# Kernel tuning notes

Hardware: AMD Instinct MI355X
Metric: run time of the kernel (lower is better)

The kernel has to match this reference:

```python
import jax, jax.numpy as jnp
import numpy as np

# Normalized sobel kernels (kornia normalize_kernel2d: divide by abs-sum = 8)
_SOBEL = np.array([
    [[-1., 0., 1.], [-2., 0., 2.], [-1., 0., 1.]],   # d/dx
    [[-1., -2., -1.], [0., 0., 0.], [1., 2., 1.]],   # d/dy
], dtype=np.float32) / 8.0
_EPS = 1e-6


def _rgb_to_grayscale(x):
    # kornia weights; x: [B,3,H,W] -> [B,1,H,W]
    return 0.299 * x[:, 0:1] + 0.587 * x[:, 1:2] + 0.114 * x[:, 2:3]


def _sobel_edges(x):
    gray = _rgb_to_grayscale(x)
    # replicate padding of 1 (kornia spatial_gradient uses replicate)
    p = jnp.pad(gray, ((0, 0), (0, 0), (1, 1), (1, 1)), mode='edge')
    k = jnp.asarray(_SOBEL)[:, None]  # [2,1,3,3] OIHW
    g = jax.lax.conv_general_dilated(
        p, k, window_strides=(1, 1), padding='VALID',
        dimension_numbers=('NCHW', 'OIHW', 'NCHW'))  # [B,2,H,W]
    # gradient magnitude: sqrt(gx^2 + gy^2 + eps)
    return jnp.sqrt(jnp.sum(g * g, axis=1, keepdims=True) + _EPS)  # [B,1,H,W]


def setup_inputs() -> dict:
    key = jax.random.key(0)
    k1, k2 = jax.random.split(key)
    shape = (16, 3, 512, 512)
    prediction = jax.random.uniform(k1, shape, dtype=jnp.float32)
    target = jax.random.uniform(k2, shape, dtype=jnp.float32)
    return {"prediction": prediction, "target": target}


def reference(prediction, target):
    # forward runs under torch.no_grad() in the original module
    pe = jax.lax.stop_gradient(_sobel_edges(prediction))
    te = jax.lax.stop_gradient(_sobel_edges(target))
    return jnp.mean(jnp.abs(pe - te))  # l1_loss, mean reduction
```

## Files before the change

kernel.cpp:

```cpp
#include <hip/hip_runtime.h>


constexpr int B = 16;
constexpr int H = 512;
constexpr int W = 512;
constexpr int TH = 32;
constexpr int TW = 64;
constexpr int HALO_H = TH + 2;
constexpr int HALO_W = TW + 2;
constexpr int NTHREADS = 256;
constexpr int TILES_W = W / TW;
constexpr int TILES_H = H / TH;
constexpr int TILES_PER_IMG = TILES_W * TILES_H;
constexpr int NBLOCKS = B * TILES_PER_IMG;
constexpr float EPS = 1e-6f;

__device__ __forceinline__ float gray_at(const float* __restrict__ img, int h, int w) {
    const float* p = img + (size_t)h * W + w;
    const size_t plane = (size_t)H * W;
    return 0.299f * p[0] + 0.587f * p[plane] + 0.114f * p[2 * plane];
}

__global__ __launch_bounds__(NTHREADS) void edge_loss_kernel(
    const float* __restrict__ pred,
    const float* __restrict__ targ,
    float* __restrict__ out)
{
    __shared__ float sp[HALO_H][HALO_W];
    __shared__ float st[HALO_H][HALO_W];

    const int bid = blockIdx.x;
    const int b   = bid / TILES_PER_IMG;
    const int t   = bid % TILES_PER_IMG;
    const int th0 = (t / TILES_W) * TH;
    const int tw0 = (t % TILES_W) * TW;
    const int tid = threadIdx.x;

    const float* __restrict__ pimg = pred + (size_t)b * 3 * H * W;
    const float* __restrict__ timg = targ + (size_t)b * 3 * H * W;

    for (int i = tid; i < HALO_H * HALO_W; i += NTHREADS) {
        const int lh = i / HALO_W;
        const int lw = i - lh * HALO_W;
        const int gh = min(max(th0 + lh - 1, 0), H - 1);
        const int gw = min(max(tw0 + lw - 1, 0), W - 1);
        sp[lh][lw] = gray_at(pimg, gh, gw);
        st[lh][lw] = gray_at(timg, gh, gw);
    }
    __syncthreads();

    float acc = 0.0f;
    #pragma unroll
    for (int r = 0; r < (TH * TW) / NTHREADS; ++r) {
        const int i  = tid + r * NTHREADS;
        const int lh = i >> 6;
        const int lw = i & 63;

        {
            const float p00 = sp[lh    ][lw], p01 = sp[lh    ][lw + 1], p02 = sp[lh    ][lw + 2];
            const float p10 = sp[lh + 1][lw],                            p12 = sp[lh + 1][lw + 2];
            const float p20 = sp[lh + 2][lw], p21 = sp[lh + 2][lw + 1], p22 = sp[lh + 2][lw + 2];
            const float gx = 0.125f * ((p02 - p00) + 2.0f * (p12 - p10) + (p22 - p20));
            const float gy = 0.125f * ((p20 - p00) + 2.0f * (p21 - p01) + (p22 - p02));
            const float pe = sqrtf(gx * gx + gy * gy + EPS);

            const float q00 = st[lh    ][lw], q01 = st[lh    ][lw + 1], q02 = st[lh    ][lw + 2];
            const float q10 = st[lh + 1][lw],                            q12 = st[lh + 1][lw + 2];
            const float q20 = st[lh + 2][lw], q21 = st[lh + 2][lw + 1], q22 = st[lh + 2][lw + 2];
            const float hx = 0.125f * ((q02 - q00) + 2.0f * (q12 - q10) + (q22 - q20));
            const float hy = 0.125f * ((q20 - q00) + 2.0f * (q21 - q01) + (q22 - q02));
            const float te = sqrtf(hx * hx + hy * hy + EPS);

            acc += fabsf(pe - te);
        }
    }

    #pragma unroll
    for (int off = 32; off > 0; off >>= 1)
        acc += __shfl_down(acc, off);

    __shared__ float wsum[NTHREADS / 64];
    if ((tid & 63) == 0) wsum[tid >> 6] = acc;
    __syncthreads();

    if (tid == 0) {
        float s = wsum[0] + wsum[1] + wsum[2] + wsum[3];
        atomicAdd(out, s * (1.0f / (float)((size_t)B * H * W)));
    }
}

extern "C" void kernel_launch(void* const* d_in, const int* in_sizes, int n_in,
                              void* d_out, int out_size, void* d_ws, size_t ws_size,
                              hipStream_t stream) {
    const float* pred = (const float*)d_in[0];
    const float* targ = (const float*)d_in[1];
    float* out = (float*)d_out;

    hipMemsetAsync(out, 0, sizeof(float), stream);
    edge_loss_kernel<<<NBLOCKS, NTHREADS, 0, stream>>>(pred, targ, out);
}
```

Before: 139.1 us.

## Vectorize halo loads with float4 and slide stencil rows in registers

Measured after the change: 134.6 us. 1.03x faster.

```diff
diff --git a/kernel.cpp b/kernel.cpp
--- a/kernel.cpp
+++ b/kernel.cpp
@@ -6,19 +6,18 @@
 constexpr int W = 512;
 constexpr int TH = 32;
 constexpr int TW = 64;
-constexpr int HALO_H = TH + 2;
-constexpr int HALO_W = TW + 2;
+constexpr int HROWS = TH + 2;
+constexpr int LSTRIDE = 72;
 constexpr int NTHREADS = 256;
 constexpr int TILES_W = W / TW;
 constexpr int TILES_H = H / TH;
 constexpr int TILES_PER_IMG = TILES_W * TILES_H;
 constexpr int NBLOCKS = B * TILES_PER_IMG;
+constexpr int NGRP = HROWS * (TW / 4);
 constexpr float EPS = 1e-6f;
 
-__device__ __forceinline__ float gray_at(const float* __restrict__ img, int h, int w) {
-    const float* p = img + (size_t)h * W + w;
-    const size_t plane = (size_t)H * W;
-    return 0.299f * p[0] + 0.587f * p[plane] + 0.114f * p[2 * plane];
+__device__ __forceinline__ float4 ldg4(const float* p) {
+    return *reinterpret_cast<const float4*>(p);
 }
 
 __global__ __launch_bounds__(NTHREADS) void edge_loss_kernel(
@@ -26,8 +25,8 @@
     const float* __restrict__ targ,
     float* __restrict__ out)
 {
-    __shared__ float sp[HALO_H][HALO_W];
-    __shared__ float st[HALO_H][HALO_W];
+    __shared__ alignas(16) float sp[HROWS][LSTRIDE];
+    __shared__ alignas(16) float st[HROWS][LSTRIDE];
 
     const int bid = blockIdx.x;
     const int b   = bid / TILES_PER_IMG;
@@ -35,44 +34,81 @@
     const int th0 = (t / TILES_W) * TH;
     const int tw0 = (t % TILES_W) * TW;
     const int tid = threadIdx.x;
+    const size_t plane = (size_t)H * W;
 
-    const float* __restrict__ pimg = pred + (size_t)b * 3 * H * W;
-    const float* __restrict__ timg = targ + (size_t)b * 3 * H * W;
+    const float* __restrict__ pimg = pred + (size_t)b * 3 * plane;
+    const float* __restrict__ timg = targ + (size_t)b * 3 * plane;
 
-    for (int i = tid; i < HALO_H * HALO_W; i += NTHREADS) {
-        const int lh = i / HALO_W;
-        const int lw = i - lh * HALO_W;
-        const int gh = min(max(th0 + lh - 1, 0), H - 1);
-        const int gw = min(max(tw0 + lw - 1, 0), W - 1);
-        sp[lh][lw] = gray_at(pimg, gh, gw);
-        st[lh][lw] = gray_at(timg, gh, gw);
+    for (int g = tid; g < NGRP; g += NTHREADS) {
+        const int row  = g >> 4;
+        const int k    = g & 15;
+        const int grow = min(max(th0 - 1 + row, 0), H - 1);
+        const float* pp = pimg + (size_t)grow * W + (tw0 + 4 * k);
+        const float* tp = timg + (size_t)grow * W + (tw0 + 4 * k);
+        const float4 pr = ldg4(pp);
+        const float4 pg = ldg4(pp + plane);
+        const float4 pb = ldg4(pp + 2 * plane);
+        const float4 tr = ldg4(tp);
+        const float4 tg = ldg4(tp + plane);
+        const float4 tb = ldg4(tp + 2 * plane);
+        float4 gp, gt;
+        gp.x = 0.299f * pr.x + 0.587f * pg.x + 0.114f * pb.x;
+        gp.y = 0.299f * pr.y + 0.587f * pg.y + 0.114f * pb.y;
+        gp.z = 0.299f * pr.z + 0.587f * pg.z + 0.114f * pb.z;
+        gp.w = 0.299f * pr.w + 0.587f * pg.w + 0.114f * pb.w;
+        gt.x = 0.299f * tr.x + 0.587f * tg.x + 0.114f * tb.x;
+        gt.y = 0.299f * tr.y + 0.587f * tg.y + 0.114f * tb.y;
+        gt.z = 0.299f * tr.z + 0.587f * tg.z + 0.114f * tb.z;
+        gt.w = 0.299f * tr.w + 0.587f * tg.w + 0.114f * tb.w;
+        *reinterpret_cast<float4*>(&sp[row][4 + 4 * k]) = gp;
+        *reinterpret_cast<float4*>(&st[row][4 + 4 * k]) = gt;
+    }
+
+    if (tid < 4 * HROWS) {
+        const int img  = tid & 1;
+        const int rr   = tid >> 1;
+        const int side = rr >= HROWS;
+        const int row  = side ? rr - HROWS : rr;
+        const int grow = min(max(th0 - 1 + row, 0), H - 1);
+        const int gcol = side ? min(tw0 + TW, W - 1) : max(tw0 - 1, 0);
+        const float* ip = (img ? timg : pimg) + (size_t)grow * W + gcol;
+        const float v = 0.299f * ip[0] + 0.587f * ip[plane] + 0.114f * ip[2 * plane];
+        float (*dst)[LSTRIDE] = img ? st : sp;
+        dst[row][side ? 68 : 3] = v;
     }
     __syncthreads();
 
+    const int lw = tid & 63;
+    const int q  = tid >> 6;
+    const int r0 = q * 8;
+    const int c0 = lw + 3, c1 = lw + 4, c2 = lw + 5;
+
+    float pa0 = sp[r0][c0],     pa1 = sp[r0][c1],     pa2 = sp[r0][c2];
+    float pb0 = sp[r0 + 1][c0], pb1 = sp[r0 + 1][c1], pb2 = sp[r0 + 1][c2];
+    float ta0 = st[r0][c0],     ta1 = st[r0][c1],     ta2 = st[r0][c2];
+    float tb0 = st[r0 + 1][c0], tb1 = st[r0 + 1][c1], tb2 = st[r0 + 1][c2];
+
     float acc = 0.0f;
     #pragma unroll
-    for (int r = 0; r < (TH * TW) / NTHREADS; ++r) {
-        const int i  = tid + r * NTHREADS;
-        const int lh = i >> 6;
-        const int lw = i & 63;
+    for (int r = 0; r < 8; ++r) {
+        const int hr = r0 + r + 2;
+        const float pc0 = sp[hr][c0], pc1 = sp[hr][c1], pc2 = sp[hr][c2];
+        const float tc0 = st[hr][c0], tc1 = st[hr][c1], tc2 = st[hr][c2];
 
-        {
-            const float p00 = sp[lh    ][lw], p01 = sp[lh    ][lw + 1], p02 = sp[lh    ][lw + 2];
-            const float p10 = sp[lh + 1][lw],                            p12 = sp[lh + 1][lw + 2];
-            const float p20 = sp[lh + 2][lw], p21 = sp[lh + 2][lw + 1], p22 = sp[lh + 2][lw + 2];
-            const float gx = 0.125f * ((p02 - p00) + 2.0f * (p12 - p10) + (p22 - p20));
-            const float gy = 0.125f * ((p20 - p00) + 2.0f * (p21 - p01) + (p22 - p02));
-            const float pe = sqrtf(gx * gx + gy * gy + EPS);
+        float gx = ((pa2 - pa0) + 2.0f * (pb2 - pb0) + (pc2 - pc0)) * 0.125f;
+        float gy = ((pc0 - pa0) + 2.0f * (pc1 - pa1) + (pc2 - pa2)) * 0.125f;
+        const float pe = sqrtf(gx * gx + gy * gy + EPS);
 
-            const float q00 = st[lh    ][lw], q01 = st[lh    ][lw + 1], q02 = st[lh    ][lw + 2];
-            const float q10 = st[lh + 1][lw],                            q12 = st[lh + 1][lw + 2];
-            const float q20 = st[lh + 2][lw], q21 = st[lh + 2][lw + 1], q22 = st[lh + 2][lw + 2];
-            const float hx = 0.125f * ((q02 - q00) + 2.0f * (q12 - q10) + (q22 - q20));
-            const float hy = 0.125f * ((q20 - q00) + 2.0f * (q21 - q01) + (q22 - q02));
-            const float te = sqrtf(hx * hx + hy * hy + EPS);
+        float hx = ((ta2 - ta0) + 2.0f * (tb2 - tb0) + (tc2 - tc0)) * 0.125f;
+        float hy = ((tc0 - ta0) + 2.0f * (tc1 - ta1) + (tc2 - ta2)) * 0.125f;
+        const float te = sqrtf(hx * hx + hy * hy + EPS);
 
-            acc += fabsf(pe - te);
-        }
+        acc += fabsf(pe - te);
+
+        pa0 = pb0; pa1 = pb1; pa2 = pb2;
+        pb0 = pc0; pb1 = pc1; pb2 = pc2;
+        ta0 = tb0; ta1 = tb1; ta2 = tb2;
+        tb0 = tc0; tb1 = tc1; tb2 = tc2;
     }
 
     #pragma unroll
@@ -84,7 +120,7 @@
     __syncthreads();
 
     if (tid == 0) {
-        float s = wsum[0] + wsum[1] + wsum[2] + wsum[3];
+        const float s = wsum[0] + wsum[1] + wsum[2] + wsum[3];
         atomicAdd(out, s * (1.0f / (float)((size_t)B * H * W)));
     }
 }
```

## Replace shared-memory tiles with register-sliding wave strips and separable Sobel

Applied to the files above, without the earlier changes.

Measured after the change: 131.3 us. 5.6% less time.

```diff
diff --git a/kernel.cpp b/kernel.cpp
--- a/kernel.cpp
+++ b/kernel.cpp
@@ -4,88 +4,153 @@
 constexpr int B = 16;
 constexpr int H = 512;
 constexpr int W = 512;
-constexpr int TH = 32;
-constexpr int TW = 64;
-constexpr int HALO_H = TH + 2;
-constexpr int HALO_W = TW + 2;
+constexpr int PLANE = H * W;
+constexpr int SR = 8;
 constexpr int NTHREADS = 256;
-constexpr int TILES_W = W / TW;
-constexpr int TILES_H = H / TH;
-constexpr int TILES_PER_IMG = TILES_W * TILES_H;
-constexpr int NBLOCKS = B * TILES_PER_IMG;
+constexpr int WAVES_PER_BLOCK = NTHREADS / 64;
+constexpr int STRIPS = B * 2 * (H / SR);
+constexpr int NBLOCKS = STRIPS / WAVES_PER_BLOCK;
 constexpr float EPS = 1e-6f;
 
-__device__ __forceinline__ float gray_at(const float* __restrict__ img, int h, int w) {
-    const float* p = img + (size_t)h * W + w;
-    const size_t plane = (size_t)H * W;
-    return 0.299f * p[0] + 0.587f * p[plane] + 0.114f * p[2 * plane];
+__device__ __forceinline__ float4 ldg4(const float* p) {
+    return *reinterpret_cast<const float4*>(p);
 }
 
-__global__ __launch_bounds__(NTHREADS) void edge_loss_kernel(
+__device__ __forceinline__ float4 gray4(float4 r, float4 g, float4 b) {
+    float4 o;
+    o.x = 0.299f * r.x + 0.587f * g.x + 0.114f * b.x;
+    o.y = 0.299f * r.y + 0.587f * g.y + 0.114f * b.y;
+    o.z = 0.299f * r.z + 0.587f * g.z + 0.114f * b.z;
+    o.w = 0.299f * r.w + 0.587f * g.w + 0.114f * b.w;
+    return o;
+}
+
+struct DS { float4 D, S; };
+
+__device__ __forceinline__ DS load_row(
+    const float* __restrict__ x0, const float* __restrict__ x1,
+    const float* __restrict__ x2,
+    int row, int col, int ecol, int lane)
+{
+    const int off = row * W + col;
+    const float4 r = ldg4(x0 + off);
+    const float4 g = ldg4(x1 + off);
+    const float4 b = ldg4(x2 + off);
+
+    float e = 0.0f;
+    if ((lane == 0) | (lane == 63)) {
+        const int eo = row * W + ecol;
+        e = 0.299f * x0[eo] + 0.587f * x1[eo] + 0.114f * x2[eo];
+    }
+
+    const float4 G = gray4(r, g, b);
+    float left  = __shfl_up(G.w, 1);
+    float right = __shfl_down(G.x, 1);
+    if (lane == 0)  left  = e;
+    if (lane == 63) right = e;
+
+    DS o;
+    o.D.x = G.y - left;
+    o.D.y = G.z - G.x;
+    o.D.z = G.w - G.y;
+    o.D.w = right - G.z;
+    o.S.x = left + 2.0f * G.x + G.y;
+    o.S.y = G.x  + 2.0f * G.y + G.z;
+    o.S.z = G.y  + 2.0f * G.z + G.w;
+    o.S.w = G.z  + 2.0f * G.w + right;
+    return o;
+}
+
+__device__ __forceinline__ float px_loss(
+    float dm, float d0, float dp, float sm, float sp,
+    float em, float e0, float ep, float qm, float qp)
+{
+    const float gx = (dm + 2.0f * d0 + dp) * 0.125f;
+    const float gy = (sp - sm) * 0.125f;
+    const float pe = sqrtf(gx * gx + gy * gy + EPS);
+    const float hx = (em + 2.0f * e0 + ep) * 0.125f;
+    const float hy = (qp - qm) * 0.125f;
+    const float te = sqrtf(hx * hx + hy * hy + EPS);
+    return fabsf(pe - te);
+}
+
+__global__ __launch_bounds__(NTHREADS, 2) void edge_loss_kernel(
     const float* __restrict__ pred,
     const float* __restrict__ targ,
-    float* __restrict__ out)
+    float* __restrict__ partial)
 {
-    __shared__ float sp[HALO_H][HALO_W];
-    __shared__ float st[HALO_H][HALO_W];
+    const int tid  = threadIdx.x;
+    const int lane = tid & 63;
+    const int s    = blockIdx.x * WAVES_PER_BLOCK + (tid >> 6);
+    const int img  = s >> 7;
+    const int half = (s >> 6) & 1;
+    const int vs   = s & 63;
+    const int r0   = vs * SR;
+    const int c0   = half * 256;
+    const int col  = c0 + 4 * lane;
+    const int ecol = (lane == 0) ? max(c0 - 1, 0) : min(c0 + 256, W - 1);
 
-    const int bid = blockIdx.x;
-    const int b   = bid / TILES_PER_IMG;
-    const int t   = bid % TILES_PER_IMG;
-    const int th0 = (t / TILES_W) * TH;
-    const int tw0 = (t % TILES_W) * TW;
-    const int tid = threadIdx.x;
+    const float* __restrict__ p0 = pred + (size_t)img * 3 * PLANE;
+    const float* __restrict__ p1 = p0 + PLANE;
+    const float* __restrict__ p2 = p0 + 2 * PLANE;
+    const float* __restrict__ t0 = targ + (size_t)img * 3 * PLANE;
+    const float* __restrict__ t1 = t0 + PLANE;
+    const float* __restrict__ t2 = t0 + 2 * PLANE;
 
-    const float* __restrict__ pimg = pred + (size_t)b * 3 * H * W;
-    const float* __restrict__ timg = targ + (size_t)b * 3 * H * W;
-
-    for (int i = tid; i < HALO_H * HALO_W; i += NTHREADS) {
-        const int lh = i / HALO_W;
-        const int lw = i - lh * HALO_W;
-        const int gh = min(max(th0 + lh - 1, 0), H - 1);
-        const int gw = min(max(tw0 + lw - 1, 0), W - 1);
-        sp[lh][lw] = gray_at(pimg, gh, gw);
-        st[lh][lw] = gray_at(timg, gh, gw);
-    }
-    __syncthreads();
+    const int rm = max(r0 - 1, 0);
+    DS pm = load_row(p0, p1, p2, rm, col, ecol, lane);
+    DS tm = load_row(t0, t1, t2, rm, col, ecol, lane);
+    DS pc = load_row(p0, p1, p2, r0, col, ecol, lane);
+    DS tc = load_row(t0, t1, t2, r0, col, ecol, lane);
 
     float acc = 0.0f;
     #pragma unroll
-    for (int r = 0; r < (TH * TW) / NTHREADS; ++r) {
-        const int i  = tid + r * NTHREADS;
-        const int lh = i >> 6;
-        const int lw = i & 63;
+    for (int r = 0; r < SR; ++r) {
+        const int rp = min(r0 + r + 1, H - 1);
+        DS pp = load_row(p0, p1, p2, rp, col, ecol, lane);
+        DS tp = load_row(t0, t1, t2, rp, col, ecol, lane);
 
-        {
-            const float p00 = sp[lh    ][lw], p01 = sp[lh    ][lw + 1], p02 = sp[lh    ][lw + 2];
-            const float p10 = sp[lh + 1][lw],                            p12 = sp[lh + 1][lw + 2];
-            const float p20 = sp[lh + 2][lw], p21 = sp[lh + 2][lw + 1], p22 = sp[lh + 2][lw + 2];
-            const float gx = 0.125f * ((p02 - p00) + 2.0f * (p12 - p10) + (p22 - p20));
-            const float gy = 0.125f * ((p20 - p00) + 2.0f * (p21 - p01) + (p22 - p02));
-            const float pe = sqrtf(gx * gx + gy * gy + EPS);
+        acc += px_loss(pm.D.x, pc.D.x, pp.D.x, pm.S.x, pp.S.x,
+                       tm.D.x, tc.D.x, tp.D.x, tm.S.x, tp.S.x);
+        acc += px_loss(pm.D.y, pc.D.y, pp.D.y, pm.S.y, pp.S.y,
+                       tm.D.y, tc.D.y, tp.D.y, tm.S.y, tp.S.y);
+        acc += px_loss(pm.D.z, pc.D.z, pp.D.z, pm.S.z, pp.S.z,
+                       tm.D.z, tc.D.z, tp.D.z, tm.S.z, tp.S.z);
+        acc += px_loss(pm.D.w, pc.D.w, pp.D.w, pm.S.w, pp.S.w,
+                       tm.D.w, tc.D.w, tp.D.w, tm.S.w, tp.S.w);
 
-            const float q00 = st[lh    ][lw], q01 = st[lh    ][lw + 1], q02 = st[lh    ][lw + 2];
-            const float q10 = st[lh + 1][lw],                            q12 = st[lh + 1][lw + 2];
-            const float q20 = st[lh + 2][lw], q21 = st[lh + 2][lw + 1], q22 = st[lh + 2][lw + 2];
-            const float hx = 0.125f * ((q02 - q00) + 2.0f * (q12 - q10) + (q22 - q20));
-            const float hy = 0.125f * ((q20 - q00) + 2.0f * (q21 - q01) + (q22 - q02));
-            const float te = sqrtf(hx * hx + hy * hy + EPS);
-
-            acc += fabsf(pe - te);
-        }
+        pm = pc; pc = pp;
+        tm = tc; tc = tp;
     }
 
     #pragma unroll
     for (int off = 32; off > 0; off >>= 1)
         acc += __shfl_down(acc, off);
 
-    __shared__ float wsum[NTHREADS / 64];
+    if (lane == 0) partial[s] = acc;
+}
+
+__global__ __launch_bounds__(256) void reduce_kernel(
+    const float* __restrict__ partial,
+    float* __restrict__ out)
+{
+    const int tid = threadIdx.x;
+    float acc = 0.0f;
+    #pragma unroll
+    for (int i = 0; i < STRIPS / 256; ++i)
+        acc += partial[tid + i * 256];
+
+    #pragma unroll
+    for (int off = 32; off > 0; off >>= 1)
+        acc += __shfl_down(acc, off);
+
+    __shared__ float wsum[4];
     if ((tid & 63) == 0) wsum[tid >> 6] = acc;
     __syncthreads();
 
     if (tid == 0) {
-        float s = wsum[0] + wsum[1] + wsum[2] + wsum[3];
-        atomicAdd(out, s * (1.0f / (float)((size_t)B * H * W)));
+        const float s = wsum[0] + wsum[1] + wsum[2] + wsum[3];
+        out[0] = s * (1.0f / (float)((size_t)B * H * W));
     }
 }
 
@@ -95,7 +160,8 @@
     const float* pred = (const float*)d_in[0];
     const float* targ = (const float*)d_in[1];
     float* out = (float*)d_out;
+    float* partial = (float*)d_ws;
 
-    hipMemsetAsync(out, 0, sizeof(float), stream);
-    edge_loss_kernel<<<NBLOCKS, NTHREADS, 0, stream>>>(pred, targ, out);
+    edge_loss_kernel<<<NBLOCKS, NTHREADS, 0, stream>>>(pred, targ, partial);
+    reduce_kernel<<<1, 256, 0, stream>>>(partial, out);
 }
```
